# Kernel optimization log

Measured on AMD Instinct MI355X. Metric: run time of the kernel, lower is better.

Reference implementation:

```python
import jax, jax.numpy as jnp
import numpy as np

B, N, DIN, DOUT = 8192, 4, 1024, 256

def setup_inputs() -> dict:
    key = jax.random.key(0)
    k1, k2, k3, k4 = jax.random.split(key, 4)
    adj = jax.random.uniform(k1, (N, N), dtype=jnp.float32)
    features = jax.random.normal(k2, (B, N, DIN), dtype=jnp.float32)
    # nn.Linear(input_size, output_size): weight [DOUT, DIN], bias [DOUT]
    bound = 1.0 / np.sqrt(DIN)
    W = jax.random.uniform(k3, (DOUT, DIN), dtype=jnp.float32, minval=-bound, maxval=bound)
    b = jax.random.uniform(k4, (DOUT,), dtype=jnp.float32, minval=-bound, maxval=bound)
    return {"adj": adj, "features": features, "W": W, "b": b}

def reference(adj, features, W, b):
    # Batched equivalent of: for i in B: linear(adj @ features[i]) -> [B, 4, DOUT]
    h = jnp.einsum("nm,bmf->bnf", adj, features)  # [B, N, DIN]
    return jnp.einsum("bnf,of->bno", h, W) + b    # [B, N, DOUT]
```

## Files before the change

kernel.cpp:

```cpp
#include <hip/hip_runtime.h>


#define DIN 1024
#define DOUT 256
#define BM 64
#define BK 64
#define KI 16
#define LDB 72
#define WS_PER_KB (DOUT * LDB)
#define A_HALFS (BM * LDB)
#define B_HALFS (DOUT * LDB)

typedef __bf16 bf16x8 __attribute__((ext_vector_type(8)));
typedef float f32x4 __attribute__((ext_vector_type(4)));
typedef unsigned short u16x8 __attribute__((ext_vector_type(8)));

__device__ __forceinline__ unsigned short f2bf(float f) {
  union { float f; unsigned int u; } v;
  v.f = f;
  unsigned int u = v.u;
  u += 0x7fffu + ((u >> 16) & 1u);
  return (unsigned short)(u >> 16);
}

__device__ __forceinline__ void glds16(const unsigned short* g, unsigned short* l) {
  __builtin_amdgcn_global_load_lds(
      (const __attribute__((address_space(1))) void*)g,
      (__attribute__((address_space(3))) void*)l, 16, 0, 0);
}

__global__ __launch_bounds__(256) void wprep_kernel(
    const float* __restrict__ W, unsigned short* __restrict__ ws) {
  const int t = blockIdx.x * 256 + threadIdx.x;
  const int col = t >> 7;
  const int k8 = t & 127;
  const int kb = k8 >> 3;
  const int kc = (k8 & 7) * 8;
  const f32x4* src = (const f32x4*)(W + (size_t)col * DIN + k8 * 8);
  f32x4 a = src[0], b = src[1];
  u16x8 pk;
#pragma unroll
  for (int m = 0; m < 4; ++m) {
    pk[m] = f2bf(a[m]);
    pk[4 + m] = f2bf(b[m]);
  }
  unsigned short* dst = ws + (size_t)kb * WS_PER_KB + col * LDB + kc;
  *(u16x8*)dst = pk;
  if ((k8 & 7) == 7) {
    u16x8 z = {0, 0, 0, 0, 0, 0, 0, 0};
    *(u16x8*)(ws + (size_t)kb * WS_PER_KB + col * LDB + 64) = z;
  }
}

__global__ __launch_bounds__(256, 2) void gconv_kernel(
    const float* __restrict__ adj, const float* __restrict__ feat,
    const unsigned short* __restrict__ wbf, const float* __restrict__ bias,
    float* __restrict__ out) {
  __shared__ __align__(16) unsigned short sB[B_HALFS];
  __shared__ __align__(16) unsigned short sA[A_HALFS];
  __shared__ float sbias[DOUT];

  const int tid = threadIdx.x;
  const int bM = blockIdx.x * BM;

  sbias[tid] = bias[tid];

  const int row0 = tid >> 3;
  const int kc0 = (tid & 7) * 8;
  const int row1 = (tid + 256) >> 3;
  const float* aptr0 = feat + (size_t)(bM + row0) * DIN + kc0;
  const float* aptr1 = feat + (size_t)(bM + row1) * DIN + kc0;
  unsigned short* sAw0 = sA + row0 * LDB + kc0;
  unsigned short* sAw1 = sA + row1 * LDB + kc0;

  const int lane = tid & 63;
  const int wid = tid >> 6;
  const int wc = wid * 64;
  const int rl = lane & 15;
  const int q = lane >> 4;

  f32x4 acc[4][4];
#pragma unroll
  for (int i = 0; i < 4; ++i)
#pragma unroll
    for (int j = 0; j < 4; ++j) acc[i][j] = f32x4{0.f, 0.f, 0.f, 0.f};

  f32x4 pa0 = *(const f32x4*)aptr0;
  f32x4 pa1 = *(const f32x4*)(aptr0 + 4);
  f32x4 pa2 = *(const f32x4*)aptr1;
  f32x4 pa3 = *(const f32x4*)(aptr1 + 4);
  aptr0 += BK;
  aptr1 += BK;

  for (int kb = 0; kb < KI; ++kb) {
    const unsigned short* bs = wbf + (size_t)kb * WS_PER_KB;
#pragma unroll
    for (int r = 0; r < 9; ++r) {
      const int idx = r * 256 + tid;
      glds16(bs + idx * 8, sB + idx * 8);
    }

    u16x8 pk0, pk1;
#pragma unroll
    for (int m = 0; m < 4; ++m) {
      pk0[m] = f2bf(pa0[m]);
      pk0[4 + m] = f2bf(pa1[m]);
      pk1[m] = f2bf(pa2[m]);
      pk1[4 + m] = f2bf(pa3[m]);
    }
    if (kb + 1 < KI) {
      pa0 = *(const f32x4*)aptr0;
      pa1 = *(const f32x4*)(aptr0 + 4);
      pa2 = *(const f32x4*)aptr1;
      pa3 = *(const f32x4*)(aptr1 + 4);
      aptr0 += BK;
      aptr1 += BK;
    }
    *(u16x8*)sAw0 = pk0;
    *(u16x8*)sAw1 = pk1;
    __syncthreads();

#pragma unroll
    for (int ks = 0; ks < 2; ++ks) {
      const int ko = ks * 32 + q * 8;
      bf16x8 af[4], bfr[4];
#pragma unroll
      for (int i = 0; i < 4; ++i)
        af[i] = *(const bf16x8*)(sA + (i * 16 + rl) * LDB + ko);
#pragma unroll
      for (int j = 0; j < 4; ++j)
        bfr[j] = *(const bf16x8*)(sB + (wc + j * 16 + rl) * LDB + ko);
#pragma unroll
      for (int i = 0; i < 4; ++i)
#pragma unroll
        for (int j = 0; j < 4; ++j)
          acc[i][j] = __builtin_amdgcn_mfma_f32_16x16x32_bf16(af[i], bfr[j],
                                                              acc[i][j], 0, 0, 0);
    }
    __syncthreads();
  }

  float am[16];
#pragma unroll
  for (int i = 0; i < 16; ++i) am[i] = adj[i];

  float bv[4];
#pragma unroll
  for (int j = 0; j < 4; ++j) bv[j] = sbias[wc + j * 16 + rl];

#pragma unroll
  for (int i = 0; i < 4; ++i) {
    const size_t rowbase = (size_t)(bM + i * 16 + q * 4);
#pragma unroll
    for (int j = 0; j < 4; ++j) {
      const int col = wc + j * 16 + rl;
      float* op = out + rowbase * DOUT + col;
      f32x4 g = acc[i][j];
#pragma unroll
      for (int n = 0; n < 4; ++n) {
        op[(size_t)n * DOUT] = am[n * 4 + 0] * g[0] + am[n * 4 + 1] * g[1] +
                               am[n * 4 + 2] * g[2] + am[n * 4 + 3] * g[3] +
                               bv[j];
      }
    }
  }
}

extern "C" void kernel_launch(void* const* d_in, const int* in_sizes, int n_in,
                              void* d_out, int out_size, void* d_ws,
                              size_t ws_size, hipStream_t stream) {
  const float* adj = (const float*)d_in[0];
  const float* feat = (const float*)d_in[1];
  const float* W = (const float*)d_in[2];
  const float* bias = (const float*)d_in[3];
  float* out = (float*)d_out;
  unsigned short* ws = (unsigned short*)d_ws;

  wprep_kernel<<<128, 256, 0, stream>>>(W, ws);
  gconv_kernel<<<8192 * 4 / BM, 256, 0, stream>>>(adj, feat, ws, bias, out);
}
```

Baseline: 219.0 us.

## Load W fragments directly from global and double-buffer A tile in LDS

```diff
diff --git a/kernel.cpp b/kernel.cpp
--- a/kernel.cpp
+++ b/kernel.cpp
@@ -6,10 +6,8 @@
 #define BM 64
 #define BK 64
 #define KI 16
-#define LDB 72
-#define WS_PER_KB (DOUT * LDB)
-#define A_HALFS (BM * LDB)
-#define B_HALFS (DOUT * LDB)
+#define LDA 72
+#define A_HALFS (BM * LDA)
 
 typedef __bf16 bf16x8 __attribute__((ext_vector_type(8)));
 typedef float f32x4 __attribute__((ext_vector_type(4)));
@@ -23,19 +21,11 @@
   return (unsigned short)(u >> 16);
 }
 
-__device__ __forceinline__ void glds16(const unsigned short* g, unsigned short* l) {
-  __builtin_amdgcn_global_load_lds(
-      (const __attribute__((address_space(1))) void*)g,
-      (__attribute__((address_space(3))) void*)l, 16, 0, 0);
-}
-
 __global__ __launch_bounds__(256) void wprep_kernel(
     const float* __restrict__ W, unsigned short* __restrict__ ws) {
   const int t = blockIdx.x * 256 + threadIdx.x;
-  const int col = t >> 7;
-  const int k8 = t & 127;
-  const int kb = k8 >> 3;
-  const int kc = (k8 & 7) * 8;
+  const int k8 = t >> 8;
+  const int col = t & 255;
   const f32x4* src = (const f32x4*)(W + (size_t)col * DIN + k8 * 8);
   f32x4 a = src[0], b = src[1];
   u16x8 pk;
@@ -44,34 +34,25 @@
     pk[m] = f2bf(a[m]);
     pk[4 + m] = f2bf(b[m]);
   }
-  unsigned short* dst = ws + (size_t)kb * WS_PER_KB + col * LDB + kc;
-  *(u16x8*)dst = pk;
-  if ((k8 & 7) == 7) {
-    u16x8 z = {0, 0, 0, 0, 0, 0, 0, 0};
-    *(u16x8*)(ws + (size_t)kb * WS_PER_KB + col * LDB + 64) = z;
-  }
+  *(u16x8*)(ws + ((size_t)k8 * 256 + col) * 8) = pk;
 }
 
 __global__ __launch_bounds__(256, 2) void gconv_kernel(
     const float* __restrict__ adj, const float* __restrict__ feat,
     const unsigned short* __restrict__ wbf, const float* __restrict__ bias,
     float* __restrict__ out) {
-  __shared__ __align__(16) unsigned short sB[B_HALFS];
-  __shared__ __align__(16) unsigned short sA[A_HALFS];
-  __shared__ float sbias[DOUT];
+  __shared__ __align__(16) unsigned short sA[2][A_HALFS];
 
   const int tid = threadIdx.x;
   const int bM = blockIdx.x * BM;
 
-  sbias[tid] = bias[tid];
-
   const int row0 = tid >> 3;
   const int kc0 = (tid & 7) * 8;
-  const int row1 = (tid + 256) >> 3;
+  const int row1 = row0 + 32;
   const float* aptr0 = feat + (size_t)(bM + row0) * DIN + kc0;
   const float* aptr1 = feat + (size_t)(bM + row1) * DIN + kc0;
-  unsigned short* sAw0 = sA + row0 * LDB + kc0;
-  unsigned short* sAw1 = sA + row1 * LDB + kc0;
+  const int sw0 = row0 * LDA + kc0;
+  const int sw1 = row1 * LDA + kc0;
 
   const int lane = tid & 63;
   const int wid = tid >> 6;
@@ -89,53 +70,68 @@
   f32x4 pa1 = *(const f32x4*)(aptr0 + 4);
   f32x4 pa2 = *(const f32x4*)aptr1;
   f32x4 pa3 = *(const f32x4*)(aptr1 + 4);
-  aptr0 += BK;
-  aptr1 += BK;
-
-  for (int kb = 0; kb < KI; ++kb) {
-    const unsigned short* bs = wbf + (size_t)kb * WS_PER_KB;
-#pragma unroll
-    for (int r = 0; r < 9; ++r) {
-      const int idx = r * 256 + tid;
-      glds16(bs + idx * 8, sB + idx * 8);
-    }
-
+  aptr0 += BK; aptr1 += BK;
+  {
     u16x8 pk0, pk1;
 #pragma unroll
     for (int m = 0; m < 4; ++m) {
-      pk0[m] = f2bf(pa0[m]);
-      pk0[4 + m] = f2bf(pa1[m]);
-      pk1[m] = f2bf(pa2[m]);
-      pk1[4 + m] = f2bf(pa3[m]);
+      pk0[m] = f2bf(pa0[m]); pk0[4 + m] = f2bf(pa1[m]);
+      pk1[m] = f2bf(pa2[m]); pk1[4 + m] = f2bf(pa3[m]);
     }
+    *(u16x8*)(sA[0] + sw0) = pk0;
+    *(u16x8*)(sA[0] + sw1) = pk1;
+  }
+  pa0 = *(const f32x4*)aptr0;
+  pa1 = *(const f32x4*)(aptr0 + 4);
+  pa2 = *(const f32x4*)aptr1;
+  pa3 = *(const f32x4*)(aptr1 + 4);
+  aptr0 += BK; aptr1 += BK;
+  __syncthreads();
+
+  const unsigned short* bbase = wbf + ((size_t)wc + rl) * 8 + (size_t)q * 256 * 8;
+
+  for (int kb = 0; kb < KI; ++kb) {
+    const int p = kb & 1;
+
+    bf16x8 bfr[2][4];
+#pragma unroll
+    for (int ks = 0; ks < 2; ++ks)
+#pragma unroll
+      for (int j = 0; j < 4; ++j)
+        bfr[ks][j] = *(const bf16x8*)(bbase +
+            ((size_t)(kb * 8 + ks * 4) * 256 + j * 16) * 8);
+
     if (kb + 1 < KI) {
-      pa0 = *(const f32x4*)aptr0;
-      pa1 = *(const f32x4*)(aptr0 + 4);
-      pa2 = *(const f32x4*)aptr1;
-      pa3 = *(const f32x4*)(aptr1 + 4);
-      aptr0 += BK;
-      aptr1 += BK;
+      u16x8 pk0, pk1;
+#pragma unroll
+      for (int m = 0; m < 4; ++m) {
+        pk0[m] = f2bf(pa0[m]); pk0[4 + m] = f2bf(pa1[m]);
+        pk1[m] = f2bf(pa2[m]); pk1[4 + m] = f2bf(pa3[m]);
+      }
+      *(u16x8*)(sA[p ^ 1] + sw0) = pk0;
+      *(u16x8*)(sA[p ^ 1] + sw1) = pk1;
+      if (kb + 2 < KI) {
+        pa0 = *(const f32x4*)aptr0;
+        pa1 = *(const f32x4*)(aptr0 + 4);
+        pa2 = *(const f32x4*)aptr1;
+        pa3 = *(const f32x4*)(aptr1 + 4);
+        aptr0 += BK; aptr1 += BK;
+      }
     }
-    *(u16x8*)sAw0 = pk0;
-    *(u16x8*)sAw1 = pk1;
-    __syncthreads();
 
 #pragma unroll
     for (int ks = 0; ks < 2; ++ks) {
       const int ko = ks * 32 + q * 8;
-      bf16x8 af[4], bfr[4];
+      bf16x8 af[4];
 #pragma unroll
       for (int i = 0; i < 4; ++i)
-        af[i] = *(const bf16x8*)(sA + (i * 16 + rl) * LDB + ko);
-#pragma unroll
-      for (int j = 0; j < 4; ++j)
-        bfr[j] = *(const bf16x8*)(sB + (wc + j * 16 + rl) * LDB + ko);
+        af[i] = *(const bf16x8*)(sA[p] + (i * 16 + rl) * LDA + ko);
 #pragma unroll
       for (int i = 0; i < 4; ++i)
 #pragma unroll
         for (int j = 0; j < 4; ++j)
-          acc[i][j] = __builtin_amdgcn_mfma_f32_16x16x32_bf16(af[i], bfr[j],
-                                                              acc[i][j], 0, 0, 0);
+          acc[i][j] = __builtin_amdgcn_mfma_f32_16x16x32_bf16(
+              af[i], bfr[ks][j], acc[i][j], 0, 0, 0);
     }
     __syncthreads();
   }
@@ -146,7 +142,7 @@
 
   float bv[4];
 #pragma unroll
-  for (int j = 0; j < 4; ++j) bv[j] = sbias[wc + j * 16 + rl];
+  for (int j = 0; j < 4; ++j) bv[j] = bias[wc + j * 16 + rl];
 
 #pragma unroll
   for (int i = 0; i < 4; ++i) {
```

Result: slower. 224.1 us (+2.3%).
